# Kernel tuning notes

Measured on AMD Instinct MI355X. Metric: run time of the kernel, lower is better.

Reference implementation:

```python
import jax, jax.numpy as jnp
import numpy as np

NUM_EXPERTS = 8
HIDDEN = 2048
FFN = 4096
TOK_PER_EXPERT = 2048
TOTAL_TOKENS = NUM_EXPERTS * TOK_PER_EXPERT


def setup_inputs() -> dict:
    key = jax.random.key(0)
    kx, k1, k2 = jax.random.split(key, 3)
    permuted_hidden_states = jax.random.normal(kx, (TOTAL_TOKENS, HIDDEN), dtype=jnp.float32)
    # Linear weights stored torch-style [out_features, in_features]
    w1 = jax.random.normal(k1, (NUM_EXPERTS, 2 * FFN, HIDDEN), dtype=jnp.float32) * (1.0 / np.sqrt(HIDDEN))
    w2 = jax.random.normal(k2, (NUM_EXPERTS, HIDDEN, FFN), dtype=jnp.float32) * (1.0 / np.sqrt(FFN))
    tokens_per_expert = jnp.full((NUM_EXPERTS,), TOK_PER_EXPERT, dtype=jnp.int64)
    return {
        "permuted_hidden_states": permuted_hidden_states,
        "tokens_per_expert": tokens_per_expert,
        "w1": w1,
        "w2": w2,
    }


def _glu(x):
    a, b = jnp.split(x, 2, axis=-1)
    return jax.nn.silu(a) * b


def reference(permuted_hidden_states, tokens_per_expert, w1, w2):
    # tokens_per_expert is a concrete host-side int array (routing metadata),
    # matching the torch module where it drives Python-level slicing.
    counts = np.asarray(tokens_per_expert)
    outs = []
    start = 0
    for i in range(counts.shape[0]):
        n = int(counts[i])
        if n == 0:
            continue
        x = permuted_hidden_states[start:start + n]          # [n, H]
        fc1 = x @ w1[i].T                                     # [n, 2*F]
        inter = _glu(fc1)                                     # [n, F]
        outs.append(inter @ w2[i].T)                          # [n, H]
        start += n
    return jnp.concatenate(outs, axis=0)
```

## Files before the change

### kernel.cpp

```cpp
#include <hip/hip_runtime.h>

#define E_NUM 8
#define HID   2048
#define FFN_  4096
#define TOK   2048

typedef __attribute__((ext_vector_type(8))) short short8;
typedef __attribute__((ext_vector_type(4))) float f32x4;

__device__ __forceinline__ short f2bf(float f) {
  unsigned u = __builtin_bit_cast(unsigned, f);
  u += 0x7fffu + ((u >> 16) & 1u);
  return (short)(u >> 16);
}

__device__ __forceinline__ void gld_lds16(const void* g, void* l) {
  __builtin_amdgcn_global_load_lds(
      (const __attribute__((address_space(1))) void*)g,
      (__attribute__((address_space(3))) void*)l, 16, 0, 0);
}

__global__ __launch_bounds__(256) void cast_f32_bf16(const float* __restrict__ s,
                                                     short* __restrict__ d, long n) {
  long idx = ((long)blockIdx.x * 256 + threadIdx.x) * 8;
  long stride = (long)gridDim.x * 256 * 8;
  for (; idx < n; idx += stride) {
    float4 v0 = *(const float4*)(s + idx);
    float4 v1 = *(const float4*)(s + idx + 4);
    short8 o;
    o[0] = f2bf(v0.x); o[1] = f2bf(v0.y); o[2] = f2bf(v0.z); o[3] = f2bf(v0.w);
    o[4] = f2bf(v1.x); o[5] = f2bf(v1.y); o[6] = f2bf(v1.z); o[7] = f2bf(v1.w);
    *(short8*)(d + idx) = o;
  }
}

__global__ __launch_bounds__(256) void cast_w1_perm(const float* __restrict__ src,
                                                    short* __restrict__ dst) {
  int b = blockIdx.x;
  int e = b >> 13;
  int rp = b & 8191;
  int q = rp >> 5, h = (rp >> 4) & 1, i = rp & 15;
  int ro = h * FFN_ + q * 16 + i;
  const float* s = src + ((size_t)e * 8192 + ro) * HID + threadIdx.x * 8;
  short* d = dst + (size_t)b * HID + threadIdx.x * 8;
  float4 v0 = *(const float4*)s;
  float4 v1 = *(const float4*)(s + 4);
  short8 o;
  o[0] = f2bf(v0.x); o[1] = f2bf(v0.y); o[2] = f2bf(v0.z); o[3] = f2bf(v0.w);
  o[4] = f2bf(v1.x); o[5] = f2bf(v1.y); o[6] = f2bf(v1.z); o[7] = f2bf(v1.w);
  *(short8*)d = o;
}


__device__ __forceinline__ short8 frag_ld(const short* tile, int sub, int lane) {
  int lr = lane & 15;
  int c = ((lane >> 4) * 8) ^ ((lr & 8) << 1);
  return *(const short8*)((const char*)tile + sub * 1024 + lr * 64 + c * 2);
}

#define RD_A4(DST, BUF, H, S)                                     \
  _Pragma("unroll") for (int mf = 0; mf < 4; mf++)                \
      DST[mf] = frag_ld(BUF, (wm * 8 + (H) + mf) * 2 + (S), lane);

#define RD_B2(DST, BUF, BB, S)                                    \
  _Pragma("unroll") for (int nf = 0; nf < 2; nf++)                \
      DST[nf] = frag_ld(BUF, (wn * 4 + (BB) + nf) * 2 + (S), lane);

#define MFMA8(H, BC, AR, BR)                                      \
  _Pragma("unroll") for (int mf = 0; mf < 4; mf++)                \
  _Pragma("unroll") for (int nf = 0; nf < 2; nf++)                \
      acc[(H) + mf][(BC) + nf] = __builtin_amdgcn_mfma_f32_16x16x32_bf16( \
          AR[mf], BR[nf], acc[(H) + mf][(BC) + nf], 0, 0, 0);

#define STAGE(BASE, TILE, H, KO) do {                                               \
    gld_lds16((BASE) + (size_t)(H) * 128 * KDIM + (KO),                             \
              (TILE) + (((H) * 8 + w) * 2 + 0) * 512);                              \
    gld_lds16((BASE) + (size_t)(H) * 128 * KDIM + (KO) + 32,                        \
              (TILE) + (((H) * 8 + w) * 2 + 1) * 512);                              \
  } while (0)

#define BAR __builtin_amdgcn_s_barrier()
#define SB  __builtin_amdgcn_sched_barrier(0)
#define P1  __builtin_amdgcn_s_setprio(1)
#define P0  __builtin_amdgcn_s_setprio(0)
#define WT_LGKM0 __builtin_amdgcn_s_waitcnt(0xC07F)
#define WT_LGKM2 __builtin_amdgcn_s_waitcnt(0xC27F)
#define WT_LGKM4 __builtin_amdgcn_s_waitcnt(0xC47F)
#define WT_VM0   __builtin_amdgcn_s_waitcnt(0x3F70)
#define WT_VM4   __builtin_amdgcn_s_waitcnt(0x3F74)

#define TILE8(TAIL, KO, ASR, ASN, BSC, BSN) do {                           \
                  \
  RD_B2(B1, BSC, 0, 0); RD_A4(Ab, ASR, 0, 1);                              \
  if ((TAIL) < 2) STAGE(Agt, ASN, 0, (KO) + 64);                           \
  SB; BAR; WT_LGKM4; SB; P1; MFMA8(0, 0, Aa, B1); P0;                      \
                                      \
  RD_B2(B3, BSC, 2, 1);                                                    \
  if ((TAIL) < 2) STAGE(Agt, ASN, 1, (KO) + 64);                           \
  SB; BAR; WT_LGKM2; SB; P1; MFMA8(0, 0, Ab, B2); P0;                      \
                                      \
  RD_B2(B4, BSC, 2, 0);                                                    \
  SB; BAR; WT_LGKM2; SB; P1; MFMA8(0, 2, Ab, B3); P0;                      \
                                      \
  RD_A4(Ab, ASR, 4, 0);                                                    \
  SB; BAR; WT_LGKM4; SB; P1; MFMA8(0, 2, Aa, B4); P0;                      \
                                      \
  RD_A4(Aa, ASR, 4, 1);                                                    \
  SB; BAR; WT_LGKM4; SB; P1; MFMA8(4, 2, Ab, B4); P0;                      \
   \
  if ((TAIL) == 0) STAGE(Bgt, BSC, 0, (KO) + 128);                         \
  SB; BAR; WT_LGKM0; SB; P1; MFMA8(4, 2, Aa, B3); P0;                      \
     \
  if ((TAIL) == 0) STAGE(Bgt, BSC, 1, (KO) + 128);                         \
  SB; BAR;                                                                  \
  if ((TAIL) == 0) { WT_VM4; } else if ((TAIL) == 1) { WT_VM0; }           \
  SB; P1; MFMA8(4, 0, Aa, B2); P0;                                         \
             \
  if ((TAIL) < 2) { RD_A4(Aa, ASN, 0, 0); RD_B2(B2, BSN, 0, 1); }          \
  SB; BAR; SB; P1; MFMA8(4, 0, Ab, B1); P0;                                \
} while (0)

template <int KDIM, bool GLU>
__global__ __launch_bounds__(512, 2) void gemm256(const short* __restrict__ A,
                                                  const short* __restrict__ B,
                                                  void* __restrict__ C, int ldc) {
  constexpr int NT = KDIM / 64;
  const int e = blockIdx.z;
  const int m0 = blockIdx.y * 256;
  const int n0 = blockIdx.x * 256;
  const int N = gridDim.x * 256;
  const int tid = threadIdx.x;
  const int w = tid >> 6, lane = tid & 63;
  const int wm = w >> 2, wn = w & 3;

  const short* Ag = A + (size_t)e * TOK * KDIM + (size_t)m0 * KDIM;
  const short* Bg = B + (size_t)e * N * KDIM + (size_t)n0 * KDIM;

  __shared__ __align__(16) short As0[16384];
  __shared__ __align__(16) short As1[16384];
  __shared__ __align__(16) short Bs0[16384];
  __shared__ __align__(16) short Bs1[16384];

  f32x4 acc[8][4] = {};
  short8 Aa[4], Ab[4], B1[2], B2[2], B3[2], B4[2];

  const int slr = lane >> 2;
  const int sclog = ((lane & 3) * 8) ^ ((slr & 8) << 1);
  const short* Agt = Ag + (size_t)(w * 16 + slr) * KDIM + sclog;
  const short* Bgt = Bg + (size_t)(w * 16 + slr) * KDIM + sclog;

  STAGE(Bgt, Bs0, 0, 0); STAGE(Bgt, Bs0, 1, 0);
  STAGE(Agt, As0, 0, 0); STAGE(Agt, As0, 1, 0);
  STAGE(Bgt, Bs1, 0, 64); STAGE(Bgt, Bs1, 1, 64);
  WT_VM4; SB; BAR;
  RD_A4(Aa, As0, 0, 0); RD_B2(B2, Bs0, 0, 1);

#pragma unroll 1
  for (int t = 0; t + 3 < NT; t += 2) {
    TILE8(0, t * 64, As0, As1, Bs0, Bs1);
    TILE8(0, (t + 1) * 64, As1, As0, Bs1, Bs0);
  }
  TILE8(1, (NT - 2) * 64, As0, As1, Bs0, Bs1);
  TILE8(2, (NT - 1) * 64, As1, As0, Bs1, Bs0);

  const int fq = lane >> 4, fr = lane & 15;
  if constexpr (GLU) {
    short* outp = (short*)C + (size_t)e * TOK * ldc;
    const int colb = (n0 >> 1) + wn * 32;
#pragma unroll
    for (int mf = 0; mf < 8; mf++)
#pragma unroll
      for (int p = 0; p < 2; p++)
#pragma unroll
        for (int r = 0; r < 4; r++) {
          int row = m0 + wm * 128 + mf * 16 + fq * 4 + r;
          int col = colb + p * 16 + fr;
          float av = acc[mf][2 * p][r];
          float bv = acc[mf][2 * p + 1][r];
          float sv = av / (1.0f + __expf(-av)) * bv;
          outp[(size_t)row * ldc + col] = f2bf(sv);
        }
  } else {
    float* outp = (float*)C + (size_t)e * TOK * ldc;
#pragma unroll
    for (int mf = 0; mf < 8; mf++)
#pragma unroll
      for (int nf = 0; nf < 4; nf++)
#pragma unroll
        for (int r = 0; r < 4; r++) {
          int row = m0 + wm * 128 + mf * 16 + fq * 4 + r;
          int col = n0 + wn * 64 + nf * 16 + fr;
          outp[(size_t)row * ldc + col] = acc[mf][nf][r];
        }
  }
}

extern "C" void kernel_launch(void* const* d_in, const int* in_sizes, int n_in,
                              void* d_out, int out_size, void* d_ws, size_t ws_size,
                              hipStream_t stream) {
  const float* x  = (const float*)d_in[0];
  const float* w1 = (const float*)d_in[2];
  const float* w2 = (const float*)d_in[3];

  const size_t W1P_BYTES   = (size_t)E_NUM * 2 * FFN_ * HID * 2;
  const size_t W2B_BYTES   = (size_t)E_NUM * HID * FFN_ * 2;
  const size_t INTER_BYTES = (size_t)E_NUM * TOK * FFN_ * 2;
  if (ws_size < W1P_BYTES + W2B_BYTES + INTER_BYTES) return;

  short* w1p   = (short*)d_ws;
  short* w2b   = (short*)((char*)d_ws + W1P_BYTES);
  short* inter = (short*)((char*)d_ws + W1P_BYTES + W2B_BYTES);
  short* xb    = (short*)d_out;
  float* out   = (float*)d_out;

  cast_f32_bf16<<<2048, 256, 0, stream>>>(x, xb, (long)E_NUM * TOK * HID);
  cast_f32_bf16<<<2048, 256, 0, stream>>>(w2, w2b, (long)E_NUM * HID * FFN_);
  cast_w1_perm<<<E_NUM * 8192, 256, 0, stream>>>(w1, w1p);

  gemm256<HID, true><<<dim3(32, 8, E_NUM), 512, 0, stream>>>(xb, w1p, (void*)inter, FFN_);
  gemm256<FFN_, false><<<dim3(8, 8, E_NUM), 512, 0, stream>>>(inter, w2b, (void*)out, HID);
}
```

Baseline: 945.7 us.

## Shrink GEMM block tile to 256x128 with 4 waves and K-step 32

Replaces the 512-thread 256x256x64 block GEMM with a 256-thread 256x128 tile using a K step of 32 and a rewritten 4-phase pipeline (TILE4) with new staging and waitcnt placement. Each wave still computes a 128x64 accumulator, but shared memory per block drops a lot and the grid doubles in N, which should raise occupancy and wave-level parallelism. In exchange, each block reuses less data, so global/L2 traffic per FLOP goes up, and the shorter K step means more barriers per unit of work. The GLU epilogue column mapping is assumed unchanged under the new tile size.

```diff
diff --git a/kernel.cpp b/kernel.cpp
--- a/kernel.cpp
+++ b/kernel.cpp
@@ -58,13 +58,13 @@
   return *(const short8*)((const char*)tile + sub * 1024 + lr * 64 + c * 2);
 }
 
-#define RD_A4(DST, BUF, H, S)                                     \
+#define RD_A4(DST, BUF, H)                                        \
   _Pragma("unroll") for (int mf = 0; mf < 4; mf++)                \
-      DST[mf] = frag_ld(BUF, (wm * 8 + (H) + mf) * 2 + (S), lane);
-
-#define RD_B2(DST, BUF, BB, S)                                    \
+      DST[mf] = frag_ld(BUF, wm * 8 + (H) + mf, lane);
+
+#define RD_B2(DST, BUF, BB)                                       \
   _Pragma("unroll") for (int nf = 0; nf < 2; nf++)                \
-      DST[nf] = frag_ld(BUF, (wn * 4 + (BB) + nf) * 2 + (S), lane);
+      DST[nf] = frag_ld(BUF, wn * 4 + (BB) + nf, lane);
 
 #define MFMA8(H, BC, AR, BR)                                      \
   _Pragma("unroll") for (int mf = 0; mf < 4; mf++)                \
@@ -72,11 +72,17 @@
       acc[(H) + mf][(BC) + nf] = __builtin_amdgcn_mfma_f32_16x16x32_bf16( \
           AR[mf], BR[nf], acc[(H) + mf][(BC) + nf], 0, 0, 0);
 
-#define STAGE(BASE, TILE, H, KO) do {                                               \
-    gld_lds16((BASE) + (size_t)(H) * 128 * KDIM + (KO),                             \
-              (TILE) + (((H) * 8 + w) * 2 + 0) * 512);                              \
-    gld_lds16((BASE) + (size_t)(H) * 128 * KDIM + (KO) + 32,                        \
-              (TILE) + (((H) * 8 + w) * 2 + 1) * 512);                              \
+#define STAGE_B(TILE, KO) do {                                              \
+    gld_lds16(Bgt + (KO),                     (TILE) + (w * 2 + 0) * 512);  \
+    gld_lds16(Bgt + (size_t)16 * KDIM + (KO), (TILE) + (w * 2 + 1) * 512);  \
+  } while (0)
+#define STAGE_A_LO(TILE, KO) do {                                           \
+    gld_lds16(Agt + (KO),                     (TILE) + (w * 4 + 0) * 512);  \
+    gld_lds16(Agt + (size_t)16 * KDIM + (KO), (TILE) + (w * 4 + 1) * 512);  \
+  } while (0)
+#define STAGE_A_HI(TILE, KO) do {                                           \
+    gld_lds16(Agt + (size_t)32 * KDIM + (KO), (TILE) + (w * 4 + 2) * 512);  \
+    gld_lds16(Agt + (size_t)48 * KDIM + (KO), (TILE) + (w * 4 + 3) * 512);  \
   } while (0)
 
 #define BAR __builtin_amdgcn_s_barrier()
@@ -84,84 +90,81 @@
 #define P1  __builtin_amdgcn_s_setprio(1)
 #define P0  __builtin_amdgcn_s_setprio(0)
 #define WT_LGKM0 __builtin_amdgcn_s_waitcnt(0xC07F)
-#define WT_LGKM2 __builtin_amdgcn_s_waitcnt(0xC27F)
 #define WT_LGKM4 __builtin_amdgcn_s_waitcnt(0xC47F)
 #define WT_VM0   __builtin_amdgcn_s_waitcnt(0x3F70)
 #define WT_VM4   __builtin_amdgcn_s_waitcnt(0x3F74)
-
-#define TILE8(TAIL, KO, ASR, ASN, BSC, BSN) do {                           \
-                  \
-  RD_B2(B1, BSC, 0, 0); RD_A4(Ab, ASR, 0, 1);                              \
-  if ((TAIL) < 2) STAGE(Agt, ASN, 0, (KO) + 64);                           \
-  SB; BAR; WT_LGKM4; SB; P1; MFMA8(0, 0, Aa, B1); P0;                      \
-                                      \
-  RD_B2(B3, BSC, 2, 1);                                                    \
-  if ((TAIL) < 2) STAGE(Agt, ASN, 1, (KO) + 64);                           \
-  SB; BAR; WT_LGKM2; SB; P1; MFMA8(0, 0, Ab, B2); P0;                      \
-                                      \
-  RD_B2(B4, BSC, 2, 0);                                                    \
-  SB; BAR; WT_LGKM2; SB; P1; MFMA8(0, 2, Ab, B3); P0;                      \
-                                      \
-  RD_A4(Ab, ASR, 4, 0);                                                    \
-  SB; BAR; WT_LGKM4; SB; P1; MFMA8(0, 2, Aa, B4); P0;                      \
-                                      \
-  RD_A4(Aa, ASR, 4, 1);                                                    \
-  SB; BAR; WT_LGKM4; SB; P1; MFMA8(4, 2, Ab, B4); P0;                      \
-   \
-  if ((TAIL) == 0) STAGE(Bgt, BSC, 0, (KO) + 128);                         \
-  SB; BAR; WT_LGKM0; SB; P1; MFMA8(4, 2, Aa, B3); P0;                      \
+#define WT_VM6   __builtin_amdgcn_s_waitcnt(0x3F76)
+
+#define TILE4(TAIL, KO, ASR, ASN, BSC, BSN, BX, BY, BXn, BYn) do {         \
+          \
+  RD_A4(Ab, ASR, 4);                                                        \
+  if ((TAIL) == 0) STAGE_B(BSC, (KO) + 64);                                \
+  SB; WT_LGKM4; SB; P1; MFMA8(0, 0, Aa, BX); P0; SB;                       \
+    \
+  if ((TAIL) == 0) { WT_VM6; } else if ((TAIL) == 1) { WT_VM4; }           \
+  BAR;                                                                      \
+  if ((TAIL) < 2) RD_B2(BXn, BSN, 0);                                      \
+  if ((TAIL) == 0) STAGE_A_LO(ASR, (KO) + 64);                             \
+  SB; P1; MFMA8(0, 2, Aa, BY); P0; SB;                                     \
+                       \
+  if ((TAIL) < 2) RD_B2(BYn, BSN, 2);                                      \
+  if ((TAIL) == 0) STAGE_A_HI(ASR, (KO) + 64);                             \
+  SB;                                                                       \
+  if ((TAIL) < 2) { WT_LGKM4; } else { WT_LGKM0; }                         \
+  SB; P1; MFMA8(4, 2, Ab, BY); P0; SB;                                     \
      \
-  if ((TAIL) == 0) STAGE(Bgt, BSC, 1, (KO) + 128);                         \
-  SB; BAR;                                                                  \
-  if ((TAIL) == 0) { WT_VM4; } else if ((TAIL) == 1) { WT_VM0; }           \
-  SB; P1; MFMA8(4, 0, Aa, B2); P0;                                         \
-             \
-  if ((TAIL) < 2) { RD_A4(Aa, ASN, 0, 0); RD_B2(B2, BSN, 0, 1); }          \
-  SB; BAR; SB; P1; MFMA8(4, 0, Ab, B1); P0;                                \
+  if ((TAIL) == 0) { WT_VM6; } else if ((TAIL) == 1) { WT_VM0; }           \
+  BAR;                                                                      \
+  if ((TAIL) < 2) RD_A4(Aa, ASN, 0);                                       \
+  SB; P1; MFMA8(4, 0, Ab, BX); P0; SB;                                     \
 } while (0)
 
 template <int KDIM, bool GLU>
-__global__ __launch_bounds__(512, 2) void gemm256(const short* __restrict__ A,
+__global__ __launch_bounds__(256, 2) void gemm128(const short* __restrict__ A,
                                                   const short* __restrict__ B,
                                                   void* __restrict__ C, int ldc) {
-  constexpr int NT = KDIM / 64;
+  constexpr int NT = KDIM / 32;
   const int e = blockIdx.z;
   const int m0 = blockIdx.y * 256;
-  const int n0 = blockIdx.x * 256;
-  const int N = gridDim.x * 256;
+  const int n0 = blockIdx.x * 128;
+  const int N = gridDim.x * 128;
   const int tid = threadIdx.x;
   const int w = tid >> 6, lane = tid & 63;
-  const int wm = w >> 2, wn = w & 3;
+  const int wm = w >> 1, wn = w & 1;
 
   const short* Ag = A + (size_t)e * TOK * KDIM + (size_t)m0 * KDIM;
   const short* Bg = B + (size_t)e * N * KDIM + (size_t)n0 * KDIM;
 
-  __shared__ __align__(16) short As0[16384];
-  __shared__ __align__(16) short As1[16384];
-  __shared__ __align__(16) short Bs0[16384];
-  __shared__ __align__(16) short Bs1[16384];
+  __shared__ __align__(16) short As0[8192];
+  __shared__ __align__(16) short As1[8192];
+  __shared__ __align__(16) short Bs0[4096];
+  __shared__ __align__(16) short Bs1[4096];
 
   f32x4 acc[8][4] = {};
   short8 Aa[4], Ab[4], B1[2], B2[2], B3[2], B4[2];
 
   const int slr = lane >> 2;
   const int sclog = ((lane & 3) * 8) ^ ((slr & 8) << 1);
-  const short* Agt = Ag + (size_t)(w * 16 + slr) * KDIM + sclog;
-  const short* Bgt = Bg + (size_t)(w * 16 + slr) * KDIM + sclog;
-
-  STAGE(Bgt, Bs0, 0, 0); STAGE(Bgt, Bs0, 1, 0);
-  STAGE(Agt, As0, 0, 0); STAGE(Agt, As0, 1, 0);
-  STAGE(Bgt, Bs1, 0, 64); STAGE(Bgt, Bs1, 1, 64);
-  WT_VM4; SB; BAR;
-  RD_A4(Aa, As0, 0, 0); RD_B2(B2, Bs0, 0, 1);
+  const short* Agt = Ag + (size_t)(w * 64 + slr) * KDIM + sclog;
+  const short* Bgt = Bg + (size_t)(w * 32 + slr) * KDIM + sclog;
+
+  STAGE_B(Bs0, 0);
+  STAGE_A_LO(As0, 0); STAGE_A_HI(As0, 0);
+  STAGE_B(Bs1, 32);
+  STAGE_A_LO(As1, 32); STAGE_A_HI(As1, 32);
+  WT_VM6; SB; BAR;
+  RD_B2(B1, Bs0, 0); SB;
+  RD_B2(B2, Bs0, 2); SB;
+  RD_A4(Aa, As0, 0); SB;
 
 #pragma unroll 1
   for (int t = 0; t + 3 < NT; t += 2) {
-    TILE8(0, t * 64, As0, As1, Bs0, Bs1);
-    TILE8(0, (t + 1) * 64, As1, As0, Bs1, Bs0);
+    TILE4(0, 0, As0, As1, Bs0, Bs1, B1, B2, B3, B4);
+    TILE4(0, 32, As1, As0, Bs1, Bs0, B3, B4, B1, B2);
+    Agt += 64; Bgt += 64;
   }
-  TILE8(1, (NT - 2) * 64, As0, As1, Bs0, Bs1);
-  TILE8(2, (NT - 1) * 64, As1, As0, Bs1, Bs0);
+  TILE4(1, 0, As0, As1, Bs0, Bs1, B1, B2, B3, B4);
+  TILE4(2, 32, As1, As0, Bs1, Bs0, B3, B4, B1, B2);
 
   const int fq = lane >> 4, fr = lane & 15;
   if constexpr (GLU) {
@@ -217,6 +220,6 @@
   cast_f32_bf16<<<2048, 256, 0, stream>>>(w2, w2b, (long)E_NUM * HID * FFN_);
   cast_w1_perm<<<E_NUM * 8192, 256, 0, stream>>>(w1, w1p);
 
-  gemm256<HID, true><<<dim3(32, 8, E_NUM), 512, 0, stream>>>(xb, w1p, (void*)inter, FFN_);
-  gemm256<FFN_, false><<<dim3(8, 8, E_NUM), 512, 0, stream>>>(inter, w2b, (void*)out, HID);
-}
+  gemm128<HID, true><<<dim3(64, 8, E_NUM), 256, 0, stream>>>(xb, w1p, (void*)inter, FFN_);
+  gemm128<FFN_, false><<<dim3(16, 8, E_NUM), 256, 0, stream>>>(inter, w2b, (void*)out, HID);
+}
```

Result: slower. 1.102 ms (+16.5%).
